# Kernel tuning notes

Hardware: AMD Instinct MI355X
Metric: run time of the kernel (lower is better)

Reference implementation:

```python
import jax, jax.numpy as jnp
import numpy as np

B, S, D = 1, 2048, 4096
H, KVH, HD = 32, 8, 128
WIN = 2048
REPEATS = H // KVH
SCALE = HD ** -0.5
NEG = -1e9


def setup_inputs() -> dict:
    key = jax.random.key(0)
    ks = jax.random.split(key, 5)
    x = jax.random.normal(ks[0], (B, S, D), dtype=jnp.float32) * 0.02
    wq = jax.random.normal(ks[1], (H * HD, D), dtype=jnp.float32) * (D ** -0.5)
    wk = jax.random.normal(ks[2], (KVH * HD, D), dtype=jnp.float32) * (D ** -0.5)
    wv = jax.random.normal(ks[3], (KVH * HD, D), dtype=jnp.float32) * (D ** -0.5)
    wo = jax.random.normal(ks[4], (H * HD, D), dtype=jnp.float32).T * ((H * HD) ** -0.5)
    wo = jnp.asarray(wo)  # [D, H*HD] torch-style (out, in) = (D, H*HD)
    positions = jnp.arange(S, dtype=jnp.int32)
    # rotary tables: freqs_cis[s, j] = exp(i * s * theta_j), theta_j = 10000^(-2j/HD)
    theta = 10000.0 ** (-jnp.arange(0, HD, 2, dtype=jnp.float32) / HD)  # [HD/2]
    ang = positions[:, None].astype(jnp.float32) * theta[None, :]       # [S, HD/2]
    freqs_cos = jnp.cos(ang)
    freqs_sin = jnp.sin(ang)
    # sliding-window causal additive mask [S, S]
    i = jnp.arange(S)[:, None]
    j = jnp.arange(S)[None, :]
    allowed = (j <= i) & (i - j < WIN)
    mask = jnp.where(allowed, 0.0, NEG).astype(jnp.float32)
    return {"x": x, "freqs_cos": freqs_cos, "freqs_sin": freqs_sin,
            "wq": wq, "wk": wk, "wv": wv, "wo": wo,
            "mask": mask, "positions": positions}


def _apply_rope(t, cos, sin):
    # t: [B, S, h, HD]; pairs are (even, odd) interleaved -> complex mul
    tr = t[..., 0::2]  # real parts [B,S,h,HD/2]
    ti = t[..., 1::2]  # imag parts
    c = cos[None, :, None, :]
    s = sin[None, :, None, :]
    out_r = tr * c - ti * s
    out_i = tr * s + ti * c
    return jnp.stack([out_r, out_i], axis=-1).reshape(t.shape)


def reference(x, freqs_cos, freqs_sin, wq, wk, wv, wo, mask, positions):
    bsz, seqlen, _ = x.shape
    q = (x @ wq.T).reshape(bsz, seqlen, H, HD)
    k = (x @ wk.T).reshape(bsz, seqlen, KVH, HD)
    v = (x @ wv.T).reshape(bsz, seqlen, KVH, HD)
    q = _apply_rope(q, freqs_cos, freqs_sin)
    k = _apply_rope(k, freqs_cos, freqs_sin)
    # GQA: repeat_interleave kv heads to match query heads (prefill path)
    k = jnp.repeat(k, REPEATS, axis=2)  # [B,S,H,HD]
    v = jnp.repeat(v, REPEATS, axis=2)
    scores = jnp.einsum("bqhd,bkhd->bhqk", q, k) * SCALE
    scores = scores + mask[None, None, :, :]
    probs = jax.nn.softmax(scores, axis=-1)
    out = jnp.einsum("bhqk,bkhd->bqhd", probs, v)
    out = out.reshape(bsz, seqlen, H * HD)
    return out @ wo.T
```

## Files before the change

### kernel.cpp

```cpp
#include <hip/hip_runtime.h>
#include <hip/hip_bf16.h>
#include <stdint.h>

#define SEQ    2048
#define DMODEL 4096
#define NH     32
#define NKVH   8
#define HDIM   128
#define KVD    (NKVH*HDIM)
#define QD     (NH*HDIM)
#define QKVN   (QD + 2*KVD)
#define ASCALE 0.08838834764831845f

typedef __attribute__((ext_vector_type(8))) short s8v;
typedef __attribute__((ext_vector_type(4))) short s4v;
typedef __attribute__((ext_vector_type(4))) float f4v;

#define MFMA16(acc, a, b) \
  asm("v_mfma_f32_16x16x32_bf16 %0, %1, %2, %0" : "+v"(acc) : "v"(a), "v"(b))

#define SBAR() do { __builtin_amdgcn_sched_barrier(0); \
                    __builtin_amdgcn_s_barrier();      \
                    __builtin_amdgcn_sched_barrier(0); } while (0)

__device__ __forceinline__ void gl2lds16(const void* g, void* l) {
  __builtin_amdgcn_global_load_lds(
      (const __attribute__((address_space(1))) void*)g,
      (__attribute__((address_space(3))) void*)l, 16, 0, 0);
}

__global__ __launch_bounds__(256) void k_cvt(const float* __restrict__ in,
                                             __hip_bfloat16* __restrict__ out, int n8,
                                             float scale) {
  int i = blockIdx.x * 256 + threadIdx.x;
  if (i >= n8) return;
  const float4* p = (const float4*)in + (size_t)i * 2;
  float4 a = p[0], b = p[1];
  union { __hip_bfloat16 h[8]; s8v v; } o;
  o.h[0] = __float2bfloat16(a.x * scale); o.h[1] = __float2bfloat16(a.y * scale);
  o.h[2] = __float2bfloat16(a.z * scale); o.h[3] = __float2bfloat16(a.w * scale);
  o.h[4] = __float2bfloat16(b.x * scale); o.h[5] = __float2bfloat16(b.y * scale);
  o.h[6] = __float2bfloat16(b.z * scale); o.h[7] = __float2bfloat16(b.w * scale);
  *(s8v*)(out + (size_t)i * 8) = o.v;
}

__global__ __launch_bounds__(256) void k_rope(__hip_bfloat16* __restrict__ t,
                                              const float* __restrict__ fc,
                                              const float* __restrict__ fs, int heads) {
  int pid = blockIdx.x * 256 + threadIdx.x;
  int i = pid & 63;
  int rest = pid >> 6;
  int h = rest % heads;
  int s = rest / heads;
  size_t base = ((size_t)s * heads + h) * HDIM + 2 * i;
  uint32_t u = *(const uint32_t*)(t + base);
  __hip_bfloat16 hh[2]; *(uint32_t*)hh = u;
  float tr = __bfloat162float(hh[0]), ti = __bfloat162float(hh[1]);
  float c = fc[(size_t)s * 64 + i], sv = fs[(size_t)s * 64 + i];
  hh[0] = __float2bfloat16(tr * c - ti * sv);
  hh[1] = __float2bfloat16(tr * sv + ti * c);
  *(uint32_t*)(t + base) = *(uint32_t*)hh;
}

__global__ __launch_bounds__(512, 2) void k_qkv(const __hip_bfloat16* __restrict__ A,
                                                const __hip_bfloat16* __restrict__ W,
                                                __hip_bfloat16* __restrict__ Qb,
                                                __hip_bfloat16* __restrict__ Kc,
                                                __hip_bfloat16* __restrict__ Vt) {
  __shared__ __align__(16) __hip_bfloat16 sm[2][256 * 64 + 192 * 64];
  const int t5 = threadIdx.x;
  const int wave = t5 >> 6, lane = t5 & 63;
  const int lrow = lane & 15, kq = lane >> 4;
  const int wm = wave >> 2, wn = wave & 3;
  const int mt = blockIdx.x & 7, nt = blockIdx.x >> 3;
  const int m0 = mt * 256, n0 = nt * 192;

  auto stageA = [&](int p, int kt) {
#pragma unroll
    for (int it = 0; it < 4; ++it) {
      int chunk = it * 512 + t5;
      int r = chunk >> 3, cc = ((chunk & 7) ^ (r & 7)) * 8;
      gl2lds16(A + (size_t)(m0 + r) * DMODEL + kt * 64 + cc,
               (char*)&sm[p][0] + it * 8192 + wave * 1024);
    }
  };
  auto stageB = [&](int p, int kt) {
#pragma unroll
    for (int it = 0; it < 3; ++it) {
      int chunk = it * 512 + t5;
      int r = chunk >> 3, cc = ((chunk & 7) ^ (r & 7)) * 8;
      gl2lds16(W + (size_t)(n0 + r) * DMODEL + kt * 64 + cc,
               (char*)&sm[p][0] + 32768 + it * 8192 + wave * 1024);
    }
  };

  f4v acc[8][3] = {};

  stageA(0, 0); stageB(0, 0);
  stageA(1, 1); stageB(1, 1);

  const int NT = DMODEL / 64;
#pragma unroll 2
  for (int t = 0; t < NT; ++t) {
    const int p = t & 1;
    const __hip_bfloat16* As = &sm[p][0];
    const __hip_bfloat16* Bs = &sm[p][256 * 64];

    __builtin_amdgcn_sched_barrier(0);
    if (t == NT - 1) asm volatile("s_waitcnt vmcnt(0)" ::: "memory");
    else             asm volatile("s_waitcnt vmcnt(7)" ::: "memory");
    __builtin_amdgcn_s_barrier();
    __builtin_amdgcn_sched_barrier(0);

    s8v a0[8], b0[3];
#pragma unroll
    for (int m = 0; m < 8; ++m) {
      int row = wm * 128 + m * 16 + lrow;
      a0[m] = *(const s8v*)&As[row * 64 + ((kq * 8) ^ ((row & 7) << 3))];
    }
#pragma unroll
    for (int n = 0; n < 3; ++n) {
      int row = wn * 48 + n * 16 + lrow;
      b0[n] = *(const s8v*)&Bs[row * 64 + ((kq * 8) ^ ((row & 7) << 3))];
    }
    __builtin_amdgcn_s_setprio(1);
#pragma unroll
    for (int m = 0; m < 4; ++m)
#pragma unroll
      for (int n = 0; n < 3; ++n) MFMA16(acc[m][n], a0[m], b0[n]);
    __builtin_amdgcn_s_setprio(0);
    SBAR();

    s8v a1[8], b1[3];
#pragma unroll
    for (int m = 0; m < 8; ++m) {
      int row = wm * 128 + m * 16 + lrow;
      a1[m] = *(const s8v*)&As[row * 64 + ((32 + kq * 8) ^ ((row & 7) << 3))];
    }
#pragma unroll
    for (int n = 0; n < 3; ++n) {
      int row = wn * 48 + n * 16 + lrow;
      b1[n] = *(const s8v*)&Bs[row * 64 + ((32 + kq * 8) ^ ((row & 7) << 3))];
    }
    __builtin_amdgcn_s_setprio(1);
#pragma unroll
    for (int m = 4; m < 8; ++m)
#pragma unroll
      for (int n = 0; n < 3; ++n) MFMA16(acc[m][n], a0[m], b0[n]);
    __builtin_amdgcn_s_setprio(0);
    SBAR();

    if (t + 2 < NT) stageA(p, t + 2);
    __builtin_amdgcn_s_setprio(1);
#pragma unroll
    for (int m = 0; m < 4; ++m)
#pragma unroll
      for (int n = 0; n < 3; ++n) MFMA16(acc[m][n], a1[m], b1[n]);
    __builtin_amdgcn_s_setprio(0);
    SBAR();

    if (t + 2 < NT) stageB(p, t + 2);
    __builtin_amdgcn_s_setprio(1);
#pragma unroll
    for (int m = 4; m < 8; ++m)
#pragma unroll
      for (int n = 0; n < 3; ++n) MFMA16(acc[m][n], a1[m], b1[n]);
    __builtin_amdgcn_s_setprio(0);
  }

#pragma unroll
  for (int m = 0; m < 8; ++m)
#pragma unroll
    for (int n = 0; n < 3; ++n) {
      int c = n0 + wn * 48 + n * 16 + lrow;
      int r0 = m0 + wm * 128 + m * 16 + kq * 4;
      if (c < QD) {
#pragma unroll
        for (int j = 0; j < 4; ++j)
          Qb[(size_t)(r0 + j) * QD + c] = __float2bfloat16(acc[m][n][j]);
      } else if (c < QD + KVD) {
#pragma unroll
        for (int j = 0; j < 4; ++j)
          Kc[(size_t)(r0 + j) * KVD + (c - QD)] = __float2bfloat16(acc[m][n][j]);
      } else {
        union { __hip_bfloat16 b[4]; s4v v; } u;
#pragma unroll
        for (int j = 0; j < 4; ++j) u.b[j] = __float2bfloat16(acc[m][n][j]);
        *(s4v*)&Vt[(size_t)(c - QD - KVD) * SEQ + r0] = u.v;
      }
    }
}

__global__ __launch_bounds__(512, 2) void k_oproj(const __hip_bfloat16* __restrict__ A,
                                                  const __hip_bfloat16* __restrict__ B,
                                                  float* __restrict__ C) {
  __shared__ __align__(16) __hip_bfloat16 sm[2][128 * 64 + 256 * 64];
  const int t5 = threadIdx.x;
  const int wave = t5 >> 6, lane = t5 & 63;
  const int lrow = lane & 15, kq = lane >> 4;
  const int wm = wave >> 2, wn = wave & 3;
  const int m0 = blockIdx.y * 128, n0 = blockIdx.x * 256;

  auto stageA = [&](int p, int kt) {
#pragma unroll
    for (int it = 0; it < 2; ++it) {
      int chunk = it * 512 + t5;
      int r = chunk >> 3, cc = ((chunk & 7) ^ (r & 7)) * 8;
      gl2lds16(A + (size_t)(m0 + r) * QD + kt * 64 + cc,
               (char*)&sm[p][0] + it * 8192 + wave * 1024);
    }
  };
  auto stageB = [&](int p, int kt) {
#pragma unroll
    for (int it = 0; it < 4; ++it) {
      int chunk = it * 512 + t5;
      int r = chunk >> 3, cc = ((chunk & 7) ^ (r & 7)) * 8;
      gl2lds16(B + (size_t)(n0 + r) * QD + kt * 64 + cc,
               (char*)&sm[p][0] + 16384 + it * 8192 + wave * 1024);
    }
  };

  f4v acc[4][4] = {};

  stageA(0, 0); stageB(0, 0);
  stageA(1, 1); stageB(1, 1);

  const int NT = QD / 64;
#pragma unroll 2
  for (int t = 0; t < NT; ++t) {
    const int p = t & 1;
    const __hip_bfloat16* As = &sm[p][0];
    const __hip_bfloat16* Bs = &sm[p][128 * 64];

    __builtin_amdgcn_sched_barrier(0);
    if (t == NT - 1) asm volatile("s_waitcnt vmcnt(0)" ::: "memory");
    else             asm volatile("s_waitcnt vmcnt(6)" ::: "memory");
    __builtin_amdgcn_s_barrier();
    __builtin_amdgcn_sched_barrier(0);

    s8v a0[4], b0[4];
#pragma unroll
    for (int m = 0; m < 4; ++m) {
      int row = wm * 64 + m * 16 + lrow;
      a0[m] = *(const s8v*)&As[row * 64 + ((kq * 8) ^ ((row & 7) << 3))];
    }
#pragma unroll
    for (int n = 0; n < 4; ++n) {
      int row = wn * 64 + n * 16 + lrow;
      b0[n] = *(const s8v*)&Bs[row * 64 + ((kq * 8) ^ ((row & 7) << 3))];
    }
    __builtin_amdgcn_s_setprio(1);
#pragma unroll
    for (int m = 0; m < 2; ++m)
#pragma unroll
      for (int n = 0; n < 4; ++n) MFMA16(acc[m][n], a0[m], b0[n]);
    __builtin_amdgcn_s_setprio(0);
    SBAR();

    s8v a1[4], b1[4];
#pragma unroll
    for (int m = 0; m < 4; ++m) {
      int row = wm * 64 + m * 16 + lrow;
      a1[m] = *(const s8v*)&As[row * 64 + ((32 + kq * 8) ^ ((row & 7) << 3))];
    }
#pragma unroll
    for (int n = 0; n < 4; ++n) {
      int row = wn * 64 + n * 16 + lrow;
      b1[n] = *(const s8v*)&Bs[row * 64 + ((32 + kq * 8) ^ ((row & 7) << 3))];
    }
    __builtin_amdgcn_s_setprio(1);
#pragma unroll
    for (int m = 2; m < 4; ++m)
#pragma unroll
      for (int n = 0; n < 4; ++n) MFMA16(acc[m][n], a0[m], b0[n]);
    __builtin_amdgcn_s_setprio(0);
    SBAR();

    if (t + 2 < NT) stageA(p, t + 2);
    __builtin_amdgcn_s_setprio(1);
#pragma unroll
    for (int m = 0; m < 2; ++m)
#pragma unroll
      for (int n = 0; n < 4; ++n) MFMA16(acc[m][n], a1[m], b1[n]);
    __builtin_amdgcn_s_setprio(0);
    SBAR();

    if (t + 2 < NT) stageB(p, t + 2);
    __builtin_amdgcn_s_setprio(1);
#pragma unroll
    for (int m = 2; m < 4; ++m)
#pragma unroll
      for (int n = 0; n < 4; ++n) MFMA16(acc[m][n], a1[m], b1[n]);
    __builtin_amdgcn_s_setprio(0);
  }

#pragma unroll
  for (int m = 0; m < 4; ++m)
#pragma unroll
    for (int n = 0; n < 4; ++n)
#pragma unroll
      for (int j = 0; j < 4; ++j) {
        int r = m0 + wm * 64 + m * 16 + kq * 4 + j;
        int c = n0 + wn * 64 + n * 16 + lrow;
        C[(size_t)r * DMODEL + c] = acc[m][n][j];
      }
}

__global__ __launch_bounds__(256, 2) void k_flash(const __hip_bfloat16* __restrict__ Q,
                                                  const __hip_bfloat16* __restrict__ Kb,
                                                  const __hip_bfloat16* __restrict__ Vtg,
                                                  __hip_bfloat16* __restrict__ O) {
  __shared__ __align__(16) __hip_bfloat16 Ks[2][64 * 128];
  __shared__ __align__(16) __hip_bfloat16 Vs[144 * 64];
  __shared__ __align__(16) __hip_bfloat16 Ps[4][16 * 64];
  const int qp = blockIdx.x, h = blockIdx.y, g = h >> 2;
  const int t = threadIdx.x, wave = t >> 6, lane = t & 63;
  const int lrow = lane & 15, kq = lane >> 4;
  const int qtA = qp, qtB = 31 - qp;

  s8v qfA[4], qfB[4];
  {
    const int qrA = qtA * 64 + wave * 16 + lrow;
    const int qrB = qtB * 64 + wave * 16 + lrow;
#pragma unroll
    for (int tt = 0; tt < 4; ++tt) {
      qfA[tt] = *(const s8v*)(Q + (size_t)qrA * QD + h * HDIM + tt * 32 + kq * 8);
      qfB[tt] = *(const s8v*)(Q + (size_t)qrB * QD + h * HDIM + tt * 32 + kq * 8);
    }
  }

  if (t < 128) {
    union { __hip_bfloat16 h8[8]; s8v v; } one;
#pragma unroll
    for (int e = 0; e < 8; ++e) one.h8[e] = __float2bfloat16(1.0f);
    *(s8v*)&Vs[128 * 64 + t * 8] = one.v;
  }

  f4v oA[9] = {}, oB[9] = {};
  float mA[4], mB[4];
#pragma unroll
  for (int j = 0; j < 4; ++j) { mA[j] = mB[j] = -1e30f; }

  auto stage_k = [&](int buf, int kv) {
#pragma unroll
    for (int it = 0; it < 4; ++it) {
      int chunk = it * 256 + t;
      int r = chunk >> 4, cc = ((chunk & 15) ^ (r & 7)) * 8;
      gl2lds16(Kb + (size_t)(kv * 64 + r) * KVD + g * HDIM + cc,
               (char*)&Ks[buf][0] + it * 4096 + wave * 1024);
    }
  };
  auto stage_v = [&](int kv) {
#pragma unroll
    for (int it = 0; it < 4; ++it) {
      int chunk = it * 256 + t;
      int d = chunk >> 3, cc = ((chunk & 7) ^ (d & 7)) * 8;
      gl2lds16(Vtg + (size_t)(g * HDIM + d) * SEQ + kv * 64 + cc,
               (char*)Vs + it * 4096 + wave * 1024);
    }
  };

  auto soft_pv = [&](f4v (&s)[4], int qt, int kv, f4v (&acc_o)[9], float (&mrun)[4]) {
    __hip_bfloat16* P = &Ps[wave][0];
    const bool diag = (kv == qt);
    asm volatile("" ::: "memory");
#pragma unroll
    for (int j = 0; j < 4; ++j) {
      float p4[4];
      float mx = -1e30f;
#pragma unroll
      for (int n = 0; n < 4; ++n) {
        float v = s[n][j];
        if (diag) {
          const int qi = qt * 64 + wave * 16 + kq * 4 + j;
          int ki = kv * 64 + n * 16 + lrow;
          if (ki > qi) v = -1e30f;
        }
        p4[n] = v;
        mx = fmaxf(mx, v);
      }
#pragma unroll
      for (int msk = 1; msk < 16; msk <<= 1) mx = fmaxf(mx, __shfl_xor(mx, msk, 64));
      if (!__all(mx <= mrun[j])) {
        float mnew = fmaxf(mrun[j], mx);
        float fsc = __expf(mrun[j] - mnew);
        mrun[j] = mnew;
#pragma unroll
        for (int n = 0; n < 9; ++n) acc_o[n][j] *= fsc;
      }
      const int drow = kq * 4 + j;
#pragma unroll
      for (int n = 0; n < 4; ++n) {
        float p = __expf(p4[n] - mrun[j]);
        P[drow * 64 + ((n * 16 + lrow) ^ ((drow & 7) << 3))] = __float2bfloat16(p);
      }
    }
    asm volatile("" ::: "memory");
#pragma unroll
    for (int tt = 0; tt < 2; ++tt) {
      s8v pa = *(const s8v*)&P[lrow * 64 + ((tt * 32 + kq * 8) ^ ((lrow & 7) << 3))];
#pragma unroll
      for (int n = 0; n < 9; ++n) {
        int d = n * 16 + lrow;
        s8v vf = *(const s8v*)&Vs[d * 64 + ((tt * 32 + kq * 8) ^ ((d & 7) << 3))];
        MFMA16(acc_o[n], pa, vf);
      }
    }
  };

  stage_k(0, 0);
  int cur = 0;
  for (int kv = 0; kv <= qtB; ++kv) {
    const bool actA = (kv <= qtA);
    __syncthreads();
    if (kv < qtB) stage_k(cur ^ 1, kv + 1);
    stage_v(kv);

    f4v sB[4] = {}, sA[4] = {};
    if (actA) {
#pragma unroll
      for (int tt = 0; tt < 4; ++tt)
#pragma unroll
        for (int n = 0; n < 4; ++n) {
          int row = n * 16 + lrow;
          s8v kf = *(const s8v*)&Ks[cur][row * 128 + ((tt * 32 + kq * 8) ^ ((row & 7) << 3))];
          MFMA16(sB[n], qfB[tt], kf);
          MFMA16(sA[n], qfA[tt], kf);
        }
    } else {
#pragma unroll
      for (int tt = 0; tt < 4; ++tt)
#pragma unroll
        for (int n = 0; n < 4; ++n) {
          int row = n * 16 + lrow;
          s8v kf = *(const s8v*)&Ks[cur][row * 128 + ((tt * 32 + kq * 8) ^ ((row & 7) << 3))];
          MFMA16(sB[n], qfB[tt], kf);
        }
    }
    __syncthreads();

    soft_pv(sB, qtB, kv, oB, mB);
    if (actA) soft_pv(sA, qtA, kv, oA, mA);
    cur ^= 1;
  }

#pragma unroll
  for (int n = 0; n < 8; ++n)
#pragma unroll
    for (int j = 0; j < 4; ++j) {
      int d = n * 16 + lrow;
      int qiB = qtB * 64 + wave * 16 + kq * 4 + j;
      O[(size_t)qiB * QD + h * HDIM + d] = __float2bfloat16(oB[n][j] / oB[8][j]);
      int qiA = qtA * 64 + wave * 16 + kq * 4 + j;
      O[(size_t)qiA * QD + h * HDIM + d] = __float2bfloat16(oA[n][j] / oA[8][j]);
    }
}

extern "C" void kernel_launch(void* const* d_in, const int* in_sizes, int n_in,
                              void* d_out, int out_size, void* d_ws, size_t ws_size,
                              hipStream_t stream) {
  const float* x  = (const float*)d_in[0];
  const float* fc = (const float*)d_in[1];
  const float* fs = (const float*)d_in[2];
  const float* wq = (const float*)d_in[3];
  const float* wk = (const float*)d_in[4];
  const float* wv = (const float*)d_in[5];
  const float* wo = (const float*)d_in[6];
  float* out = (float*)d_out;

  char* ws = (char*)d_ws;
  auto alloc = [&](size_t bytes) {
    char* p = ws;
    ws += (bytes + 255) & ~(size_t)255;
    return p;
  };
  __hip_bfloat16* xb  = (__hip_bfloat16*)alloc((size_t)SEQ * DMODEL * 2);
  __hip_bfloat16* wf  = (__hip_bfloat16*)alloc((size_t)QKVN * DMODEL * 2);
  __hip_bfloat16* wob = (__hip_bfloat16*)alloc((size_t)DMODEL * QD * 2);
  __hip_bfloat16* Qb  = (__hip_bfloat16*)alloc((size_t)SEQ * QD * 2);
  __hip_bfloat16* Kc  = (__hip_bfloat16*)alloc((size_t)SEQ * KVD * 2);
  __hip_bfloat16* Vtg = (__hip_bfloat16*)alloc((size_t)KVD * SEQ * 2);
  __hip_bfloat16* Ob  = (__hip_bfloat16*)alloc((size_t)SEQ * QD * 2);

  auto cvt = [&](const float* src, __hip_bfloat16* dst, size_t n, float scale) {
    int n8 = (int)(n / 8);
    k_cvt<<<dim3((n8 + 255) / 256), dim3(256), 0, stream>>>(src, dst, n8, scale);
  };
  cvt(x,  xb, (size_t)SEQ * DMODEL, 1.0f);
  cvt(wq, wf, (size_t)QD * DMODEL, ASCALE);
  cvt(wk, wf + (size_t)QD * DMODEL, (size_t)KVD * DMODEL, 1.0f);
  cvt(wv, wf + (size_t)(QD + KVD) * DMODEL, (size_t)KVD * DMODEL, 1.0f);
  cvt(wo, wob, (size_t)DMODEL * QD, 1.0f);

  k_qkv<<<dim3(256), dim3(512), 0, stream>>>(xb, wf, Qb, Kc, Vtg);

  k_rope<<<dim3(SEQ * NH * 64 / 256), 256, 0, stream>>>(Qb, fc, fs, NH);
  k_rope<<<dim3(SEQ * NKVH * 64 / 256), 256, 0, stream>>>(Kc, fc, fs, NKVH);

  k_flash<<<dim3(16, NH), 256, 0, stream>>>(Qb, Kc, Vtg, Ob);

  k_oproj<<<dim3(DMODEL / 256, SEQ / 128), dim3(512), 0, stream>>>(Ob, wob, out);
}
```

Baseline: 294.9 us.

## Merge five conversion launches into one and transpose score MFMA operands in flash kernel

Replaces the five separate fp32-to-bf16 conversion launches with a single kernel that picks its source tensor by index range, which removes launch overhead and tail gaps between the launches. The flash-attention kernel also swaps the MFMA operand order, so each lane holds the scores for a single query row. That lets the row max be reduced with two shuffles instead of four, keeps one running max per lane, and writes P with packed 4-element stores. Rescale factors are now broadcast with __shfl, which adds some cross-lane work in exchange.

```diff
diff --git a/kernel.cpp b/kernel.cpp
--- a/kernel.cpp
+++ b/kernel.cpp
@@ -29,19 +29,31 @@
       (__attribute__((address_space(3))) void*)l, 16, 0, 0);
 }
 
-__global__ __launch_bounds__(256) void k_cvt(const float* __restrict__ in,
-                                             __hip_bfloat16* __restrict__ out, int n8,
-                                             float scale) {
+__global__ __launch_bounds__(256) void k_cvt5(const float* __restrict__ x,
+                                              const float* __restrict__ wq,
+                                              const float* __restrict__ wk,
+                                              const float* __restrict__ wv,
+                                              const float* __restrict__ wo,
+                                              __hip_bfloat16* __restrict__ xb,
+                                              __hip_bfloat16* __restrict__ wf,
+                                              __hip_bfloat16* __restrict__ wob) {
   int i = blockIdx.x * 256 + threadIdx.x;
-  if (i >= n8) return;
-  const float4* p = (const float4*)in + (size_t)i * 2;
+  const float* src;
+  __hip_bfloat16* dst;
+  float scale = 1.0f;
+  if (i < 1048576)       { src = x;  dst = xb; }
+  else if (i < 3145728)  { src = wq; dst = wf;  i -= 1048576; scale = ASCALE; }
+  else if (i < 3670016)  { src = wk; dst = wf + (size_t)QD * DMODEL;  i -= 3145728; }
+  else if (i < 4194304)  { src = wv; dst = wf + (size_t)(QD + KVD) * DMODEL; i -= 3670016; }
+  else                   { src = wo; dst = wob; i -= 4194304; }
+  const float4* p = (const float4*)src + (size_t)i * 2;
   float4 a = p[0], b = p[1];
   union { __hip_bfloat16 h[8]; s8v v; } o;
   o.h[0] = __float2bfloat16(a.x * scale); o.h[1] = __float2bfloat16(a.y * scale);
   o.h[2] = __float2bfloat16(a.z * scale); o.h[3] = __float2bfloat16(a.w * scale);
   o.h[4] = __float2bfloat16(b.x * scale); o.h[5] = __float2bfloat16(b.y * scale);
   o.h[6] = __float2bfloat16(b.z * scale); o.h[7] = __float2bfloat16(b.w * scale);
-  *(s8v*)(out + (size_t)i * 8) = o.v;
+  *(s8v*)(dst + (size_t)i * 8) = o.v;
 }
 
 __global__ __launch_bounds__(256) void k_rope(__hip_bfloat16* __restrict__ t,
@@ -337,9 +349,7 @@
   }
 
   f4v oA[9] = {}, oB[9] = {};
-  float mA[4], mB[4];
-#pragma unroll
-  for (int j = 0; j < 4; ++j) { mA[j] = mB[j] = -1e30f; }
+  float mA = -1e30f, mB = -1e30f;
 
   auto stage_k = [&](int buf, int kv) {
 #pragma unroll
@@ -360,45 +370,52 @@
     }
   };
 
-  auto soft_pv = [&](f4v (&s)[4], int qt, int kv, f4v (&acc_o)[9], float (&mrun)[4]) {
+  auto soft_pv = [&](f4v (&s)[4], int qt, int kv, f4v (&acc_o)[9], float& mrun) {
     __hip_bfloat16* P = &Ps[wave][0];
     const bool diag = (kv == qt);
-    asm volatile("" ::: "memory");
-#pragma unroll
-    for (int j = 0; j < 4; ++j) {
-      float p4[4];
-      float mx = -1e30f;
-#pragma unroll
-      for (int n = 0; n < 4; ++n) {
+    const int qi = qt * 64 + wave * 16 + lrow;
+    const int swz = (lrow & 7) << 3;
+    float pv[4][4];
+    float mx = -1e30f;
+#pragma unroll
+    for (int n = 0; n < 4; ++n)
+#pragma unroll
+      for (int j = 0; j < 4; ++j) {
         float v = s[n][j];
         if (diag) {
-          const int qi = qt * 64 + wave * 16 + kq * 4 + j;
-          int ki = kv * 64 + n * 16 + lrow;
+          int ki = kv * 64 + n * 16 + kq * 4 + j;
           if (ki > qi) v = -1e30f;
         }
-        p4[n] = v;
+        pv[n][j] = v;
         mx = fmaxf(mx, v);
       }
-#pragma unroll
-      for (int msk = 1; msk < 16; msk <<= 1) mx = fmaxf(mx, __shfl_xor(mx, msk, 64));
-      if (!__all(mx <= mrun[j])) {
-        float mnew = fmaxf(mrun[j], mx);
-        float fsc = __expf(mrun[j] - mnew);
-        mrun[j] = mnew;
-#pragma unroll
-        for (int n = 0; n < 9; ++n) acc_o[n][j] *= fsc;
+    mx = fmaxf(mx, __shfl_xor(mx, 16, 64));
+    mx = fmaxf(mx, __shfl_xor(mx, 32, 64));
+    if (!__all(mx <= mrun)) {
+      float mnew = fmaxf(mrun, mx);
+      float fsc = __expf(mrun - mnew);
+      mrun = mnew;
+      float fj[4];
+#pragma unroll
+      for (int j = 0; j < 4; ++j) fj[j] = __shfl(fsc, kq * 4 + j, 64);
+#pragma unroll
+      for (int n = 0; n < 9; ++n) {
+        acc_o[n][0] *= fj[0]; acc_o[n][1] *= fj[1];
+        acc_o[n][2] *= fj[2]; acc_o[n][3] *= fj[3];
       }
-      const int drow = kq * 4 + j;
-#pragma unroll
-      for (int n = 0; n < 4; ++n) {
-        float p = __expf(p4[n] - mrun[j]);
-        P[drow * 64 + ((n * 16 + lrow) ^ ((drow & 7) << 3))] = __float2bfloat16(p);
-      }
     }
     asm volatile("" ::: "memory");
 #pragma unroll
+    for (int n = 0; n < 4; ++n) {
+      union { __hip_bfloat16 b[4]; s4v v; } u;
+#pragma unroll
+      for (int j = 0; j < 4; ++j) u.b[j] = __float2bfloat16(__expf(pv[n][j] - mrun));
+      *(s4v*)&P[lrow * 64 + ((n * 16 + kq * 4) ^ swz)] = u.v;
+    }
+    asm volatile("" ::: "memory");
+#pragma unroll
     for (int tt = 0; tt < 2; ++tt) {
-      s8v pa = *(const s8v*)&P[lrow * 64 + ((tt * 32 + kq * 8) ^ ((lrow & 7) << 3))];
+      s8v pa = *(const s8v*)&P[lrow * 64 + ((tt * 32 + kq * 8) ^ swz)];
 #pragma unroll
       for (int n = 0; n < 9; ++n) {
         int d = n * 16 + lrow;
@@ -424,8 +441,8 @@
         for (int n = 0; n < 4; ++n) {
           int row = n * 16 + lrow;
           s8v kf = *(const s8v*)&Ks[cur][row * 128 + ((tt * 32 + kq * 8) ^ ((row & 7) << 3))];
-          MFMA16(sB[n], qfB[tt], kf);
-          MFMA16(sA[n], qfA[tt], kf);
+          MFMA16(sB[n], kf, qfB[tt]);
+          MFMA16(sA[n], kf, qfA[tt]);
         }
     } else {
 #pragma unroll
@@ -434,7 +451,7 @@
         for (int n = 0; n < 4; ++n) {
           int row = n * 16 + lrow;
           s8v kf = *(const s8v*)&Ks[cur][row * 128 + ((tt * 32 + kq * 8) ^ ((row & 7) << 3))];
-          MFMA16(sB[n], qfB[tt], kf);
+          MFMA16(sB[n], kf, qfB[tt]);
         }
     }
     __syncthreads();
@@ -482,15 +499,7 @@
   __hip_bfloat16* Vtg = (__hip_bfloat16*)alloc((size_t)KVD * SEQ * 2);
   __hip_bfloat16* Ob  = (__hip_bfloat16*)alloc((size_t)SEQ * QD * 2);
 
-  auto cvt = [&](const float* src, __hip_bfloat16* dst, size_t n, float scale) {
-    int n8 = (int)(n / 8);
-    k_cvt<<<dim3((n8 + 255) / 256), dim3(256), 0, stream>>>(src, dst, n8, scale);
-  };
-  cvt(x,  xb, (size_t)SEQ * DMODEL, 1.0f);
-  cvt(wq, wf, (size_t)QD * DMODEL, ASCALE);
-  cvt(wk, wf + (size_t)QD * DMODEL, (size_t)KVD * DMODEL, 1.0f);
-  cvt(wv, wf + (size_t)(QD + KVD) * DMODEL, (size_t)KVD * DMODEL, 1.0f);
-  cvt(wo, wob, (size_t)DMODEL * QD, 1.0f);
+  k_cvt5<<<dim3(24576), dim3(256), 0, stream>>>(x, wq, wk, wv, wo, xb, wf, wob);
 
   k_qkv<<<dim3(256), dim3(512), 0, stream>>>(xb, wf, Qb, Kc, Vtg);
 
```

After: 277.5 us. 5.9% less time.
